# Optimization experiments

Measured on AMD Instinct MI355X. Metric: run time of the kernel, lower is better.

## Reference

```python
import jax, jax.numpy as jnp
import numpy as np

# dims
P = 512          # perception_vector_size
A_DIM = 64       # action_vector_size
D_MODEL = 256
D_STATE = 16
D_CONV = 4
D_INNER = 2 * D_MODEL      # expand=2 -> 512
DT_RANK = D_MODEL // 16    # ceil(256/16) = 16
BATCH = 8192


def setup_inputs() -> dict:
    key = jax.random.key(0)
    ks = jax.random.split(key, 12)
    s = lambda k, shp, sc=0.02: (jax.random.normal(k, shp, jnp.float32) * sc)
    return {
        "perception": jax.random.normal(ks[0], (BATCH, P), jnp.float32),
        # Brain linears
        "W_in": s(ks[1], (D_MODEL, P)), "b_in": jnp.zeros((D_MODEL,), jnp.float32),
        "mu_w": s(ks[2], (A_DIM, D_MODEL)), "mu_b": jnp.zeros((A_DIM,), jnp.float32),
        "ls_w": s(ks[3], (A_DIM, D_MODEL)), "ls_b": jnp.zeros((A_DIM,), jnp.float32),
        # Mamba params (mamba_ssm Mamba(d_model=256, d_state=16, d_conv=4, expand=2))
        "in_proj_w": s(ks[4], (2 * D_INNER, D_MODEL)),            # no bias
        "conv_w": s(ks[5], (D_INNER, D_CONV), 0.1),               # depthwise causal conv
        "conv_b": jnp.zeros((D_INNER,), jnp.float32),
        "x_proj_w": s(ks[6], (DT_RANK + 2 * D_STATE, D_INNER)),   # no bias
        "dt_proj_w": s(ks[7], (D_INNER, DT_RANK), 0.1),
        "dt_proj_b": s(ks[8], (D_INNER,), 0.1),
        # S4D real init: A_log[d, n] = log(n+1)
        "A_log": jnp.log(jnp.broadcast_to(jnp.arange(1, D_STATE + 1, dtype=jnp.float32), (D_INNER, D_STATE))),
        "Dskip": jnp.ones((D_INNER,), jnp.float32),
        "out_proj_w": s(ks[9], (D_MODEL, D_INNER)),               # no bias
    }


def _mamba(x, in_proj_w, conv_w, conv_b, x_proj_w, dt_proj_w, dt_proj_b, A_log, Dskip):
    # x: [B, L, d_model]
    Bsz, L, _ = x.shape
    xz = x @ in_proj_w.T                       # [B, L, 2*D_INNER]
    u, z = jnp.split(xz, 2, axis=-1)           # each [B, L, D_INNER]
    # causal depthwise conv1d (padding d_conv-1 on the left), then SiLU
    u_pad = jnp.pad(u, ((0, 0), (D_CONV - 1, 0), (0, 0)))
    idx = jnp.arange(L)[:, None] + jnp.arange(D_CONV)[None, :]   # [L, K]
    windows = u_pad[:, idx, :]                 # [B, L, K, D_INNER]
    u = jnp.einsum('blkc,ck->blc', windows, conv_w) + conv_b
    u = jax.nn.silu(u)
    # input-dependent SSM params
    x_dbl = u @ x_proj_w.T                     # [B, L, dt_rank + 2*d_state]
    dt, Bm, Cm = jnp.split(x_dbl, [DT_RANK, DT_RANK + D_STATE], axis=-1)
    delta = jax.nn.softplus(dt @ dt_proj_w.T + dt_proj_b)  # [B, L, D_INNER]
    A = -jnp.exp(A_log)                        # [D_INNER, D_STATE]

    def step(h, inp):
        u_t, dl, b_t, c_t = inp                # [B,D],[B,D],[B,N],[B,N]
        dA = jnp.exp(dl[..., None] * A)        # [B, D, N]
        h = dA * h + dl[..., None] * b_t[:, None, :] * u_t[..., None]
        y = jnp.einsum('bdn,bn->bd', h, c_t)
        return h, y

    h0 = jnp.zeros((Bsz, D_INNER, D_STATE), u.dtype)
    xs = (u.transpose(1, 0, 2), delta.transpose(1, 0, 2),
          Bm.transpose(1, 0, 2), Cm.transpose(1, 0, 2))
    _, ys = jax.lax.scan(step, h0, xs)         # ys: [L, B, D_INNER]
    y = ys.transpose(1, 0, 2) + Dskip * u      # skip connection D*u
    return y * jax.nn.silu(z)


def reference(perception, W_in, b_in, mu_w, mu_b, ls_w, ls_b,
              in_proj_w, conv_w, conv_b, x_proj_w, dt_proj_w, dt_proj_b,
              A_log, Dskip, out_proj_w):
    x = (perception @ W_in.T + b_in)[:, None, :]     # [B, 1, d_model]
    y = _mamba(x, in_proj_w, conv_w, conv_b, x_proj_w,
               dt_proj_w, dt_proj_b, A_log, Dskip)   # [B, 1, D_INNER]
    h = (y @ out_proj_w.T)[:, 0, :]                  # [B, d_model]
    mu = jnp.tanh(h @ mu_w.T + mu_b)
    log_std = jnp.clip(h @ ls_w.T + ls_b, -5.0, 2.0)
    return mu, log_std
```

## Files before the change

### kernel.cpp

```cpp
#include <hip/hip_runtime.h>
#include <hip/hip_fp16.h>
#include <cmath>

#define BATCH 8192

typedef short bf16x8 __attribute__((ext_vector_type(8)));
typedef float f32x4 __attribute__((ext_vector_type(4)));
typedef float f32x16 __attribute__((ext_vector_type(16)));

__device__ __forceinline__ void split2(float x, unsigned short& h, unsigned short& l){
    unsigned u = __float_as_uint(x);
    unsigned hr = u + 0x7fffu + ((u >> 16) & 1u);
    unsigned short hs = (unsigned short)(hr >> 16);
    float hf = __uint_as_float(((unsigned)hs) << 16);
    float d = x - hf;
    unsigned v = __float_as_uint(d);
    unsigned short ls = (unsigned short)((v + 0x7fffu + ((v >> 16) & 1u)) >> 16);
    h = hs; l = ls;
}
__device__ __forceinline__ float fsig(float x){ return 1.f / (1.f + __expf(-x)); }
__device__ __forceinline__ float ftanh(float x){
    x = fminf(fmaxf(x, -10.f), 10.f);
    const float e = __expf(2.f*x);
    return (e - 1.f) / (e + 1.f);
}
__device__ __forceinline__ void async_copy16(void* lds, const void* g){
    __builtin_amdgcn_global_load_lds(
        (const __attribute__((address_space(1))) unsigned int*)g,
        (__attribute__((address_space(3))) unsigned int*)lds, 16, 0, 0);
}


__global__ __launch_bounds__(256) void prep_all(
    const float* __restrict__ percep,
    const float* __restrict__ in_proj, const float* __restrict__ W_in,
    const float* __restrict__ b_in,
    const float* __restrict__ mu_w, const float* __restrict__ ls_w,
    const float* __restrict__ conv_w, const float* __restrict__ conv_b,
    const float* __restrict__ out_proj, const float* __restrict__ x_proj,
    unsigned short* __restrict__ W1h, unsigned short* __restrict__ W1l,
    unsigned short* __restrict__ Wth, unsigned short* __restrict__ Wtl,
    unsigned short* __restrict__ Xph, unsigned short* __restrict__ Xpl,
    unsigned short* __restrict__ Ph, unsigned short* __restrict__ Pl,
    float* __restrict__ b1)
{
    __shared__ float As[16][68];
    __shared__ float Ws[16][68];
    __shared__ unsigned short Lh[4096];
    __shared__ unsigned short Ll[4096];

    const int bx = blockIdx.x, by = blockIdx.y;
    const int tid = threadIdx.x;
    if (bx >= 20){
        const int s = (bx-20)*8 + by;
        const int band = s >> 4, ks = s & 15;
        const size_t tbase = (size_t)s*4096;
#pragma unroll
        for (int g=0; g<2; ++g){
            const int u = g*256 + tid;
            const int row = u >> 2, piece = u & 3;
            const float* src = percep + (size_t)(band*128 + row)*512 + ks*32 + piece*8;
            const float4 v0 = *reinterpret_cast<const float4*>(src);
            const float4 v1 = *reinterpret_cast<const float4*>(src+4);
            unsigned short h[8], l[8];
            split2(v0.x,h[0],l[0]); split2(v0.y,h[1],l[1]);
            split2(v0.z,h[2],l[2]); split2(v0.w,h[3],l[3]);
            split2(v1.x,h[4],l[4]); split2(v1.y,h[5],l[5]);
            split2(v1.z,h[6],l[6]); split2(v1.w,h[7],l[7]);
            uint4 H, L;
            H.x=(unsigned)h[0]|((unsigned)h[1]<<16); H.y=(unsigned)h[2]|((unsigned)h[3]<<16);
            H.z=(unsigned)h[4]|((unsigned)h[5]<<16); H.w=(unsigned)h[6]|((unsigned)h[7]<<16);
            L.x=(unsigned)l[0]|((unsigned)l[1]<<16); L.y=(unsigned)l[2]|((unsigned)l[3]<<16);
            L.z=(unsigned)l[4]|((unsigned)l[5]<<16); L.w=(unsigned)l[6]|((unsigned)l[7]<<16);
            const int off = piece*1024 + row*8;
            *reinterpret_cast<uint4*>(&Lh[off]) = H;
            *reinterpret_cast<uint4*>(&Ll[off]) = L;
        }
        __syncthreads();
#pragma unroll
        for (int g=0; g<2; ++g){
            const int f = g*256 + tid;
            *reinterpret_cast<uint4*>(&Ph[tbase + f*8]) = *reinterpret_cast<const uint4*>(&Lh[f*8]);
            *reinterpret_cast<uint4*>(&Pl[tbase + f*8]) = *reinterpret_cast<const uint4*>(&Ll[f*8]);
        }
        return;
    }
    if (bx == 18){
        const int lane = tid & 63, w = tid >> 6;
        const float4 bv = *reinterpret_cast<const float4*>(&b_in[lane*4]);
        const int nbase = by*128 + w*32;
#pragma unroll 4
        for (int i=0;i<32;i++){
            const int n = nbase + i;
            const float4 av = *reinterpret_cast<const float4*>(&in_proj[(size_t)n*256 + lane*4]);
            float p = av.x*bv.x + av.y*bv.y + av.z*bv.z + av.w*bv.w;
#pragma unroll
            for (int off=32; off; off>>=1) p += __shfl_xor(p, off, 64);
            if (lane == 0)
                b1[n] = (n < 512) ? fmaf(p, conv_w[n*4+3], conv_b[n]) : p;
        }
        return;
    }
    if (bx == 19){
        const int c0 = by*64;
#pragma unroll
        for (int p=0;p<16;p++){
            const int idx = p*256 + tid;
            const int rrow = idx >> 6;
            const int c = c0 + (idx & 63);
            const float v = (rrow < 48) ? x_proj[(size_t)rrow*512 + c] : 0.f;
            unsigned short h,l; split2(v,h,l);
            const int ks = c >> 5, r = (c >> 3) & 3, pos = c & 7;
            const size_t off = (size_t)ks*2048 + (r*64 + rrow)*8 + pos;
            Xph[off]=h; Xpl[off]=l;
        }
        return;
    }
    const float* A; unsigned short *Oh, *Ol; int m0; bool wt;
    const float* B;
    if (bx < 16){ A = in_proj + (size_t)bx*64*256; B = W_in; Oh=W1h; Ol=W1l; m0=bx*64; wt=false; }
    else { A = (bx==16 ? mu_w : ls_w); B = out_proj; Oh=Wth; Ol=Wtl; m0=(bx-16)*64; wt=true; }
    const int n0 = by*64;

    const int tm = tid/16, tn = tid%16;
    float acc[4][4];
#pragma unroll
    for (int i=0;i<4;i++)
#pragma unroll
      for (int j=0;j<4;j++) acc[i][j]=0.f;

    for (int k0=0;k0<256;k0+=16){
        {
            const int kf = tid & 3, mm = tid >> 2;
            float4 v = *reinterpret_cast<const float4*>(A + (size_t)mm*256 + k0 + kf*4);
            As[kf*4+0][mm]=v.x; As[kf*4+1][mm]=v.y; As[kf*4+2][mm]=v.z; As[kf*4+3][mm]=v.w;
        }
        {
            const int nn4 = tid & 15, kk = tid >> 4;
            float4 v = *reinterpret_cast<const float4*>(B + (size_t)(k0+kk)*512 + n0 + nn4*4);
            *reinterpret_cast<float4*>(&Ws[kk][nn4*4]) = v;
        }
        __syncthreads();
#pragma unroll
        for (int k=0;k<16;k++){
            const float4 av = *reinterpret_cast<const float4*>(&As[k][tm*4]);
            const float4 bv = *reinterpret_cast<const float4*>(&Ws[k][tn*4]);
            float a[4]={av.x,av.y,av.z,av.w}, b[4]={bv.x,bv.y,bv.z,bv.w};
#pragma unroll
            for (int i=0;i<4;i++)
#pragma unroll
                for (int j=0;j<4;j++) acc[i][j] = fmaf(a[i], b[j], acc[i][j]);
        }
        __syncthreads();
    }
#pragma unroll
    for (int i=0;i<4;i++){
        const int gm = m0 + tm*4 + i;
        const float s = (!wt && gm < 512) ? conv_w[gm*4+3] : 1.f;
        const int n = n0 + tn*4;
        unsigned short h[4], l[4];
#pragma unroll
        for (int j=0;j<4;j++) split2(acc[i][j]*s, h[j], l[j]);
        const int ks = n >> 5, r = (n >> 3) & 3, pos = n & 7;
        size_t off;
        if (wt) off = (size_t)ks*4096 + (r*128 + gm)*8 + pos;
        else    off = (size_t)((gm>>7)*16 + ks)*4096 + (r*128 + (gm&127))*8 + pos;
        *reinterpret_cast<ushort4*>(&Oh[off]) = make_ushort4(h[0],h[1],h[2],h[3]);
        *reinterpret_cast<ushort4*>(&Ol[off]) = make_ushort4(l[0],l[1],l[2],l[3]);
    }
}

__global__ __launch_bounds__(256,2) void mgemm5(
    const unsigned short* __restrict__ AhT, const unsigned short* __restrict__ AlT,
    const unsigned short* __restrict__ BhT, const unsigned short* __restrict__ BlT,
    const float* __restrict__ bias,
    float* __restrict__ O0, __half* __restrict__ O1)
{
    constexpr int TM=128, TN=128, WM=64, WN=64;
    constexpr int WAVES_N = TN/WN;
    constexpr int MT = WM/32, NT = WN/32;
    constexpr int PL = 4096;
    constexpr int BUF = 4*PL;
    constexpr int NK = 16;
    __shared__ unsigned short sm[2*BUF];

    const int tid = threadIdx.x;
    const int mb = blockIdx.x, nb = blockIdx.y;
    const int m0 = mb * TM, n0 = nb * TN;
    const int lane = tid & 63, wid = tid >> 6;
    const int half = lane >> 5, l32 = lane & 31;
    const int wm = (wid / WAVES_N) * WM;
    const int wn = (wid % WAVES_N) * WN;

    f32x16 acc[MT][NT];
#pragma unroll
    for (int i=0;i<MT;i++)
#pragma unroll
      for (int j=0;j<NT;j++)
#pragma unroll
        for (int r=0;r<16;r++) acc[i][j][r] = 0.f;

    auto dmaAll = [&](int k, int b){
        unsigned short* base = sm + b*BUF;
        const unsigned short* Ah = AhT + (size_t)(mb*16 + k)*PL;
        const unsigned short* Al = AlT + (size_t)(mb*16 + k)*PL;
        const unsigned short* Bh = BhT + (size_t)(nb*16 + k)*PL;
        const unsigned short* Bl = BlT + (size_t)(nb*16 + k)*PL;
#pragma unroll
        for (int it=0; it<2; ++it){
            const int f = it*256 + tid;
            const int wb = (it*256 + wid*64)*8;
            async_copy16(base +        wb, Ah + f*8);
            async_copy16(base +   PL + wb, Al + f*8);
            async_copy16(base + 2*PL + wb, Bh + f*8);
            async_copy16(base + 3*PL + wb, Bl + f*8);
        }
    };

    dmaAll(0, 0);

    for (int k=0; k<NK; ++k){
        const int cur = k & 1, nxt = cur ^ 1;
        __syncthreads();
        if (k+1 < NK) dmaAll(k+1, nxt);

        const unsigned short* bufc = sm + cur*BUF;
        bf16x8 ah[2][MT], al[2][MT], bh[2][NT], bl[2][NT];
#pragma unroll
        for (int j=0;j<2;j++){
            const int r = j*2 + half;
#pragma unroll
            for (int mt=0; mt<MT; ++mt){
                const int off = (r*TM + wm + mt*32 + l32)*8;
                ah[j][mt] = *reinterpret_cast<const bf16x8*>(&bufc[off]);
                al[j][mt] = *reinterpret_cast<const bf16x8*>(&bufc[PL + off]);
            }
#pragma unroll
            for (int nt=0; nt<NT; ++nt){
                const int off = (r*TN + wn + nt*32 + l32)*8;
                bh[j][nt] = *reinterpret_cast<const bf16x8*>(&bufc[2*PL + off]);
                bl[j][nt] = *reinterpret_cast<const bf16x8*>(&bufc[3*PL + off]);
            }
        }
#pragma unroll
        for (int j=0;j<2;j++){
#pragma unroll
            for (int mt=0; mt<MT; ++mt)
#pragma unroll
            for (int nt=0; nt<NT; ++nt)
                acc[mt][nt] = __builtin_amdgcn_mfma_f32_32x32x16_bf16(ah[j][mt], bh[j][nt], acc[mt][nt], 0,0,0);
#pragma unroll
            for (int mt=0; mt<MT; ++mt)
#pragma unroll
            for (int nt=0; nt<NT; ++nt)
                acc[mt][nt] = __builtin_amdgcn_mfma_f32_32x32x16_bf16(al[j][mt], bh[j][nt], acc[mt][nt], 0,0,0);
#pragma unroll
            for (int mt=0; mt<MT; ++mt)
#pragma unroll
            for (int nt=0; nt<NT; ++nt)
                acc[mt][nt] = __builtin_amdgcn_mfma_f32_32x32x16_bf16(ah[j][mt], bl[j][nt], acc[mt][nt], 0,0,0);
        }
    }

#pragma unroll
    for (int mt=0; mt<MT; ++mt)
#pragma unroll
    for (int nt=0; nt<NT; ++nt)
#pragma unroll
    for (int r=0; r<16; ++r){
        const int row = m0 + wm + mt*32 + (r&3) + 8*(r>>2) + 4*half;
        const int col = n0 + wn + nt*32 + l32;
        float v = acc[mt][nt][r] + bias[col];
        if (col < 512) O0[(size_t)row*512 + col] = v * fsig(v);
        else           O1[(size_t)row*512 + (col-512)] = __float2half(v);
    }
}

__global__ __launch_bounds__(256,2) void tail_fused3(
    const float* __restrict__ Uf, const __half* __restrict__ Zh,
    const unsigned short* __restrict__ XphT, const unsigned short* __restrict__ XplT,
    const unsigned short* __restrict__ WthT, const unsigned short* __restrict__ WtlT,
    const float* __restrict__ dtw, const float* __restrict__ dtb,
    const float* __restrict__ dskip,
    const float* __restrict__ mu_b, const float* __restrict__ ls_b,
    float* __restrict__ mu_o, float* __restrict__ ls_o)
{
    constexpr int TM = 16;
    constexpr int ROWB = 136;
    __shared__ unsigned short sYh[2][16*ROWB];
    __shared__ unsigned short sYl[2][16*ROWB];
    __shared__ float sxd[TM][49];
    __shared__ float sBC[TM];

    const int tid = threadIdx.x;
    const int m0 = blockIdx.x * TM;
    const int lane = tid & 63, wid = tid >> 6;
    const int quad = lane >> 4, l16 = lane & 15;
    const int q = wid;

    float2 uvp[4][4]; __half2 zvp[4][4];
#pragma unroll
    for (int c=0;c<4;++c){
        const int d0 = c*128 + 2*lane;
#pragma unroll
        for (int rr=0; rr<4; ++rr){
            const size_t off = (size_t)(m0 + q*4 + rr)*512 + d0;
            uvp[c][rr] = *reinterpret_cast<const float2*>(&Uf[off]);
            zvp[c][rr] = *reinterpret_cast<const __half2*>(&Zh[off]);
        }
    }
    float2 dbp[4], dkp[4];
#pragma unroll
    for (int c=0;c<4;++c){
        const int d0 = c*128 + 2*lane;
        dbp[c] = *reinterpret_cast<const float2*>(&dtb[d0]);
        dkp[c] = *reinterpret_cast<const float2*>(&dskip[d0]);
    }

    f32x4 acc = (f32x4){0.f,0.f,0.f,0.f};
    const float* arow = Uf + (size_t)(m0 + l16)*512 + quad*8;
    const int bxp = (quad*64 + wid*16 + l16)*8;
#pragma unroll
    for (int k=0; k<16; ++k){
        const float4 a0 = *reinterpret_cast<const float4*>(arow + k*32);
        const float4 a1 = *reinterpret_cast<const float4*>(arow + k*32 + 4);
        const bf16x8 bh = *reinterpret_cast<const bf16x8*>(&XphT[(size_t)k*2048 + bxp]);
        const bf16x8 bl = *reinterpret_cast<const bf16x8*>(&XplT[(size_t)k*2048 + bxp]);
        bf16x8 ah, al;
        {
            const float a[8] = {a0.x,a0.y,a0.z,a0.w,a1.x,a1.y,a1.z,a1.w};
            unsigned short h[8], l[8];
#pragma unroll
            for (int j=0;j<8;j++) split2(a[j], h[j], l[j]);
#pragma unroll
            for (int j=0;j<8;j++){ ah[j] = (short)h[j]; al[j] = (short)l[j]; }
        }
        acc = __builtin_amdgcn_mfma_f32_16x16x32_bf16(ah, bh, acc, 0,0,0);
        acc = __builtin_amdgcn_mfma_f32_16x16x32_bf16(al, bh, acc, 0,0,0);
        acc = __builtin_amdgcn_mfma_f32_16x16x32_bf16(ah, bl, acc, 0,0,0);
    }

    {
        const int colp = wid*16 + l16;
        if (colp < 48){
#pragma unroll
            for (int r=0;r<4;++r) sxd[quad*4 + r][colp] = acc[r];
        }
    }
    __syncthreads();
    if (tid < TM){
        float bc = 0.f;
#pragma unroll
        for (int n=0;n<16;n++) bc = fmaf(sxd[tid][16+n], sxd[tid][32+n], bc);
        sBC[tid] = bc;
    }
    __syncthreads();

    f32x4 oacc[2];
    oacc[0] = (f32x4){0.f,0.f,0.f,0.f};
    oacc[1] = (f32x4){0.f,0.f,0.f,0.f};

    const unsigned ybase = (unsigned)(lane >> 2)*68 + (unsigned)(lane & 3);

#pragma unroll
    for (int c=0; c<4; ++c){
        const int d0 = c*128 + 2*lane, d1 = d0 + 1;
        float w0[16], w1[16];
#pragma unroll
        for (int j=0;j<4;j++){
            const float4 a = *reinterpret_cast<const float4*>(&dtw[d0*16 + j*4]);
            w0[j*4]=a.x; w0[j*4+1]=a.y; w0[j*4+2]=a.z; w0[j*4+3]=a.w;
            const float4 b = *reinterpret_cast<const float4*>(&dtw[d1*16 + j*4]);
            w1[j*4]=b.x; w1[j*4+1]=b.y; w1[j*4+2]=b.z; w1[j*4+3]=b.w;
        }
        const float db0 = dbp[c].x, db1 = dbp[c].y;
        const float dk0 = dkp[c].x, dk1 = dkp[c].y;

        unsigned short* yh = sYh[c&1];
        unsigned short* yl = sYl[c&1];
#pragma unroll
        for (int rr=0; rr<4; ++rr){
            const int r = q*4 + rr;
            float xr[16];
#pragma unroll
            for (int j=0;j<16;j++) xr[j] = sxd[r][j];
            const float bc = sBC[r];
            float t0 = db0, t1 = db1;
#pragma unroll
            for (int j=0;j<16;j++){ t0 = fmaf(xr[j], w0[j], t0); t1 = fmaf(xr[j], w1[j], t1); }
            const float dl0 = (t0 > 20.f) ? t0 : __logf(1.f + __expf(t0));
            const float dl1 = (t1 > 20.f) ? t1 : __logf(1.f + __expf(t1));
            const float2 uv = uvp[c][rr];
            const __half2 zv = zvp[c][rr];
            const float z0 = __low2float(zv), z1 = __high2float(zv);
            const float y0 = uv.x * fmaf(dl0, bc, dk0) * (z0 * fsig(z0));
            const float y1 = uv.y * fmaf(dl1, bc, dk1) * (z1 * fsig(z1));
            unsigned short h0,l0,h1,l1;
            split2(y0,h0,l0); split2(y1,h1,l1);
            reinterpret_cast<unsigned*>(yh)[ybase + r*4] = (unsigned)h0 | ((unsigned)h1<<16);
            reinterpret_cast<unsigned*>(yl)[ybase + r*4] = (unsigned)l0 | ((unsigned)l1<<16);
        }
        __syncthreads();

#pragma unroll
        for (int s=0; s<4; ++s){
            const int kt = c*4 + s;
            const int aoff = (4*s + quad)*ROWB + l16*8;
            const bf16x8 ya = *reinterpret_cast<const bf16x8*>(&yh[aoff]);
            const bf16x8 yl8 = *reinterpret_cast<const bf16x8*>(&yl[aoff]);
            bf16x8 bh2[2], bl2[2];
#pragma unroll
            for (int nt=0; nt<2; ++nt){
                const size_t boff = (size_t)kt*4096 + (quad*128 + wid*32 + nt*16 + l16)*8;
                bh2[nt] = *reinterpret_cast<const bf16x8*>(&WthT[boff]);
                bl2[nt] = *reinterpret_cast<const bf16x8*>(&WtlT[boff]);
            }
#pragma unroll
            for (int nt=0; nt<2; ++nt)
                oacc[nt] = __builtin_amdgcn_mfma_f32_16x16x32_bf16(ya, bh2[nt], oacc[nt], 0,0,0);
#pragma unroll
            for (int nt=0; nt<2; ++nt)
                oacc[nt] = __builtin_amdgcn_mfma_f32_16x16x32_bf16(yl8, bh2[nt], oacc[nt], 0,0,0);
#pragma unroll
            for (int nt=0; nt<2; ++nt)
                oacc[nt] = __builtin_amdgcn_mfma_f32_16x16x32_bf16(ya, bl2[nt], oacc[nt], 0,0,0);
        }
    }

#pragma unroll
    for (int nt=0; nt<2; ++nt)
#pragma unroll
    for (int r=0; r<4; ++r){
        const int row = m0 + quad*4 + r;
        const int col = wid*32 + nt*16 + l16;
        const float v = oacc[nt][r];
        if (col < 64) mu_o[(size_t)row*64 + col] = ftanh(v + mu_b[col]);
        else          ls_o[(size_t)row*64 + (col-64)] = fminf(fmaxf(v + ls_b[col-64], -5.f), 2.f);
    }
}

extern "C" void kernel_launch(void* const* d_in, const int* in_sizes, int n_in,
                              void* d_out, int out_size, void* d_ws, size_t ws_size,
                              hipStream_t stream) {
    (void)in_sizes; (void)n_in; (void)out_size; (void)ws_size;
    const float* percep  = (const float*)d_in[0];
    const float* W_in    = (const float*)d_in[1];
    const float* b_in    = (const float*)d_in[2];
    const float* mu_w    = (const float*)d_in[3];
    const float* mu_b    = (const float*)d_in[4];
    const float* ls_w    = (const float*)d_in[5];
    const float* ls_b    = (const float*)d_in[6];
    const float* in_proj = (const float*)d_in[7];
    const float* conv_w  = (const float*)d_in[8];
    const float* conv_b  = (const float*)d_in[9];
    const float* x_proj  = (const float*)d_in[10];
    const float* dt_w    = (const float*)d_in[11];
    const float* dt_b    = (const float*)d_in[12];
    const float* Dskip   = (const float*)d_in[14];
    const float* out_proj= (const float*)d_in[15];

    char* ws = (char*)d_ws;
    const size_t MB = 1u<<20;
    unsigned short* W1h = (unsigned short*)(ws);
    unsigned short* W1l = (unsigned short*)(ws + 1*MB);
    unsigned short* Wth = (unsigned short*)(ws + 2*MB);
    unsigned short* Wtl = (unsigned short*)(ws + 2*MB + 128*1024);
    unsigned short* Xph = (unsigned short*)(ws + 2*MB + 256*1024);
    unsigned short* Xpl = (unsigned short*)(ws + 2*MB + 320*1024);
    float*          b1  = (float*)         (ws + 2*MB + 384*1024);
    unsigned short* Ph  = (unsigned short*)(ws + 4*MB);
    unsigned short* Pl  = (unsigned short*)(ws + 12*MB);
    float*          Uf  = (float*)         (ws + 20*MB);
    __half*         Zh  = (__half*)        (ws + 36*MB);

    float* mu_o = (float*)d_out;
    float* ls_o = (float*)d_out + (size_t)BATCH*64;

    dim3 blk(256);
    prep_all<<<dim3(148,8), blk, 0, stream>>>(
        percep, in_proj, W_in, b_in, mu_w, ls_w, conv_w, conv_b, out_proj, x_proj,
        W1h, W1l, Wth, Wtl, Xph, Xpl, Ph, Pl, b1);
    mgemm5<<<dim3(64,8), blk, 0, stream>>>(
        Ph, Pl, W1h, W1l, b1, Uf, Zh);
    tail_fused3<<<dim3(BATCH/16), blk, 0, stream>>>(
        Uf, Zh, Xph, Xpl, Wth, Wtl, dt_w, dt_b, Dskip, mu_b, ls_b, mu_o, ls_o);
}
```

Measured before the change: 170.4 us.

## Drop LDS double-buffering in split-bf16 GEMM, load fragments directly from global

The GEMM kernel no longer stages A/B hi/lo tiles into shared memory with async copies and a double buffer. Each wave now reads its MFMA fragments straight from the pre-tiled global layout, with the k-loop fully unrolled and no barriers. This removes LDS traffic and __syncthreads, but each wave re-fetches tiles that neighbouring waves also read, relying on L1/L2 to absorb the redundant loads. Overlap now comes only from compiler scheduling of the global loads.

```diff
diff --git a/kernel.cpp b/kernel.cpp
--- a/kernel.cpp
+++ b/kernel.cpp
@@ -170,7 +170,7 @@
     }
 }
 
-__global__ __launch_bounds__(256,2) void mgemm5(
+__global__ __launch_bounds__(256,2) void mgemm6(
     const unsigned short* __restrict__ AhT, const unsigned short* __restrict__ AlT,
     const unsigned short* __restrict__ BhT, const unsigned short* __restrict__ BlT,
     const float* __restrict__ bias,
@@ -180,9 +180,7 @@
     constexpr int WAVES_N = TN/WN;
     constexpr int MT = WM/32, NT = WN/32;
     constexpr int PL = 4096;
-    constexpr int BUF = 4*PL;
     constexpr int NK = 16;
-    __shared__ unsigned short sm[2*BUF];
 
     const int tid = threadIdx.x;
     const int mb = blockIdx.x, nb = blockIdx.y;
@@ -200,31 +198,18 @@
 #pragma unroll
         for (int r=0;r<16;r++) acc[i][j][r] = 0.f;
 
-    auto dmaAll = [&](int k, int b){
-        unsigned short* base = sm + b*BUF;
-        const unsigned short* Ah = AhT + (size_t)(mb*16 + k)*PL;
-        const unsigned short* Al = AlT + (size_t)(mb*16 + k)*PL;
-        const unsigned short* Bh = BhT + (size_t)(nb*16 + k)*PL;
-        const unsigned short* Bl = BlT + (size_t)(nb*16 + k)*PL;
-#pragma unroll
-        for (int it=0; it<2; ++it){
-            const int f = it*256 + tid;
-            const int wb = (it*256 + wid*64)*8;
-            async_copy16(base +        wb, Ah + f*8);
-            async_copy16(base +   PL + wb, Al + f*8);
-            async_copy16(base + 2*PL + wb, Bh + f*8);
-            async_copy16(base + 3*PL + wb, Bl + f*8);
-        }
-    };
-
-    dmaAll(0, 0);
-
+    const unsigned short* Ah0 = AhT + (size_t)mb*NK*PL;
+    const unsigned short* Al0 = AlT + (size_t)mb*NK*PL;
+    const unsigned short* Bh0 = BhT + (size_t)nb*NK*PL;
+    const unsigned short* Bl0 = BlT + (size_t)nb*NK*PL;
+
+#pragma unroll
     for (int k=0; k<NK; ++k){
-        const int cur = k & 1, nxt = cur ^ 1;
-        __syncthreads();
-        if (k+1 < NK) dmaAll(k+1, nxt);
-
-        const unsigned short* bufc = sm + cur*BUF;
+        const unsigned short* ap = Ah0 + k*PL;
+        const unsigned short* alp = Al0 + k*PL;
+        const unsigned short* bp = Bh0 + k*PL;
+        const unsigned short* blp = Bl0 + k*PL;
+
         bf16x8 ah[2][MT], al[2][MT], bh[2][NT], bl[2][NT];
 #pragma unroll
         for (int j=0;j<2;j++){
@@ -232,14 +217,14 @@
 #pragma unroll
             for (int mt=0; mt<MT; ++mt){
                 const int off = (r*TM + wm + mt*32 + l32)*8;
-                ah[j][mt] = *reinterpret_cast<const bf16x8*>(&bufc[off]);
-                al[j][mt] = *reinterpret_cast<const bf16x8*>(&bufc[PL + off]);
+                ah[j][mt] = *reinterpret_cast<const bf16x8*>(&ap[off]);
+                al[j][mt] = *reinterpret_cast<const bf16x8*>(&alp[off]);
             }
 #pragma unroll
             for (int nt=0; nt<NT; ++nt){
                 const int off = (r*TN + wn + nt*32 + l32)*8;
-                bh[j][nt] = *reinterpret_cast<const bf16x8*>(&bufc[2*PL + off]);
-                bl[j][nt] = *reinterpret_cast<const bf16x8*>(&bufc[3*PL + off]);
+                bh[j][nt] = *reinterpret_cast<const bf16x8*>(&bp[off]);
+                bl[j][nt] = *reinterpret_cast<const bf16x8*>(&blp[off]);
             }
         }
 #pragma unroll
@@ -480,7 +465,7 @@
     prep_all<<<dim3(148,8), blk, 0, stream>>>(
         percep, in_proj, W_in, b_in, mu_w, ls_w, conv_w, conv_b, out_proj, x_proj,
         W1h, W1l, Wth, Wtl, Xph, Xpl, Ph, Pl, b1);
-    mgemm5<<<dim3(64,8), blk, 0, stream>>>(
+    mgemm6<<<dim3(64,8), blk, 0, stream>>>(
         Ph, Pl, W1h, W1l, b1, Uf, Zh);
     tail_fused3<<<dim3(BATCH/16), blk, 0, stream>>>(
         Uf, Zh, Xph, Xpl, Wth, Wtl, dt_w, dt_b, Dskip, mu_b, ls_b, mu_o, ls_o);
```

Result: no change. 169.6 us (-0.5%).
